# Kernel tuning notes

Hardware: AMD Instinct MI355X
Metric: run time of the kernel (lower is better)

Reference implementation:

```python
import jax, jax.numpy as jnp
import numpy as np

N, E, C, K = 50000, 800000, 64, 8
D = C * K  # 512
NEG_SLOPE = 0.01  # torch leaky_relu default


def setup_inputs() -> dict:
    key = jax.random.key(0)
    ks = jax.random.split(key, 6)
    x = jax.random.normal(ks[0], (N, D), dtype=jnp.float32)
    edge_index = jax.random.randint(ks[1], (2, E), 0, N, dtype=jnp.int64)
    conv_W = jax.random.normal(ks[2], (K, C, C), dtype=jnp.float32) * (1.0 / np.sqrt(C))
    conv_b = jax.random.normal(ks[3], (K, C), dtype=jnp.float32) * 0.01
    W1 = jax.random.normal(ks[4], (D, D), dtype=jnp.float32) * (1.0 / np.sqrt(D))
    W2 = jax.random.normal(ks[5], (D, D), dtype=jnp.float32) * (1.0 / np.sqrt(D))
    return {"x": x, "edge_index": edge_index, "conv_W": conv_W,
            "conv_b": conv_b, "W1": W1, "W2": W2}


def _gcn_conv(xk, Wk, bk, src, dst, dinv, n):
    # PyG GCNConv: transform, then symmetric-normalized aggregation with self-loops,
    # then add bias.
    xt = xk @ Wk.T  # [N, C]
    norm = dinv[src] * dinv[dst]  # [E]
    agg = jax.ops.segment_sum(norm[:, None] * xt[src], dst, num_segments=n)
    agg = agg + (dinv * dinv)[:, None] * xt  # self-loop contribution
    return agg + bk


def reference(x, edge_index, conv_W, conv_b, W1, W2):
    n = x.shape[0]
    src, dst = edge_index[0], edge_index[1]
    # degree with self-loops (edge weight 1)
    deg = jax.ops.segment_sum(jnp.ones((E,), x.dtype), dst, num_segments=n) + 1.0
    dinv = deg ** -0.5
    xr = x.reshape(n, C, K)
    zs = [jax.nn.leaky_relu(_gcn_conv(xr[:, :, i], conv_W[i], conv_b[i], src, dst, dinv, n),
                            negative_slope=NEG_SLOPE)
          for i in range(K)]
    z = jnp.concatenate(zs, axis=1)  # [N, D]
    z = jax.nn.leaky_relu(z, negative_slope=NEG_SLOPE)
    # dropout is identity in eval mode (dr=12 is invalid for torch Dropout anyway)
    z_fc1 = z @ W1.T
    z_fc2 = z @ W2.T
    s = jnp.sum(z_fc1.T @ z_fc2, axis=0)  # [D]
    # softmax over axis 0 of a [1, D] tensor (as in the original code)
    gate = jax.nn.softmax((s / jnp.sqrt(jnp.asarray(D, x.dtype)))[None, :], axis=0)
    return z * gate
```

## Files before the change

### kernel.cpp

```cpp
#include <hip/hip_runtime.h>

#define NN 50000
#define EE 800000
#define KK 8
#define DD 512
#define CAP 64
#define FILL_BLOCKS ((EE + 255) / 256)
#define LROW 520

typedef __attribute__((ext_vector_type(8))) short short8;
typedef __attribute__((ext_vector_type(4))) float f32x4;
typedef __attribute__((ext_vector_type(4))) unsigned u32x4;

__device__ __forceinline__ float leaky2(float v) {
    v = (v < 0.0f) ? 0.01f * v : v;
    v = (v < 0.0f) ? 0.01f * v : v;
    return v;
}

__device__ __forceinline__ unsigned short f2bf(float f) {
    unsigned u = __float_as_uint(f);
    u += 0x7fffu + ((u >> 16) & 1u);
    return (unsigned short)(u >> 16);
}
__device__ __forceinline__ float bf_lo(unsigned u) { return __uint_as_float(u << 16); }
__device__ __forceinline__ float bf_hi(unsigned u) { return __uint_as_float(u & 0xffff0000u); }

__device__ __forceinline__ void add8(float acc[8], u32x4 v) {
    acc[0] += bf_lo(v[0]); acc[1] += bf_hi(v[0]);
    acc[2] += bf_lo(v[1]); acc[3] += bf_hi(v[1]);
    acc[4] += bf_lo(v[2]); acc[5] += bf_hi(v[2]);
    acc[6] += bf_lo(v[3]); acc[7] += bf_hi(v[3]);
}

__global__ void k_fill_wconv(const int* __restrict__ ei, int* __restrict__ cursor,
                             unsigned short* __restrict__ bw,
                             const float* __restrict__ W,
                             unsigned short* __restrict__ Wbf) {
    int b = blockIdx.x;
    if (b < FILL_BLOCKS) {
        int e = b * 256 + threadIdx.x;
        if (e < EE) {
            int s = ei[e];
            int d = ei[EE + e];
            int p = atomicAdd(&cursor[d], 1);
            if (p < CAP) bw[(size_t)d * CAP + p] = (unsigned short)s;
        }
    } else {
        int i = (b - FILL_BLOCKS) * 256 + threadIdx.x;
        if (i < KK * 64 * 64) Wbf[i] = f2bf(W[i]);
    }
}

__global__ __launch_bounds__(256) void k_transform(const float* __restrict__ x,
                                                   const unsigned short* __restrict__ Wbf,
                                                   const int* __restrict__ cnt,
                                                   unsigned short* __restrict__ xt) {
    __shared__ unsigned short lxT[32 * LROW];
    const int t = threadIdx.x;
    const int n0 = blockIdx.x * 32;

    const f32x4* x4 = (const f32x4*)x;
    #pragma unroll
    for (int i = 0; i < 16; i++) {
        int idx = i * 256 + t;
        int n = idx >> 7;
        int q = idx & 127;
        int n_eff = n0 + n; if (n_eff >= NN) n_eff = NN - 1;
        f32x4 v = __builtin_nontemporal_load(&x4[(size_t)n_eff * 128 + q]);
        int c = q >> 1;
        int k0 = (q & 1) * 4;
        unsigned short* p = &lxT[n * LROW + k0 * 64 + c];
        p[0] = f2bf(v[0]); p[64] = f2bf(v[1]); p[128] = f2bf(v[2]); p[192] = f2bf(v[3]);
    }
    __syncthreads();

    const int wv   = t >> 6;
    const int lane = t & 63;
    const int l15  = lane & 15;
    const int quad = lane >> 4;
    const f32x4 zero = {0.f, 0.f, 0.f, 0.f};

    #pragma unroll
    for (int kk = 0; kk < 2; kk++) {
        const int k = wv * 2 + kk;
        short8 afr[4][2];
        #pragma unroll
        for (int jt = 0; jt < 4; jt++)
            #pragma unroll
            for (int ks = 0; ks < 2; ks++)
                afr[jt][ks] = *(const short8*)&Wbf[k * 4096 + (jt * 16 + l15) * 64 + ks * 32 + quad * 8];

        #pragma unroll
        for (int ng = 0; ng < 2; ng++) {
            short8 bfr[2];
            #pragma unroll
            for (int ks = 0; ks < 2; ks++)
                bfr[ks] = *(const short8*)&lxT[(ng * 16 + l15) * LROW + k * 64 + ks * 32 + quad * 8];
            f32x4 acc[4];
            #pragma unroll
            for (int jt = 0; jt < 4; jt++) {
                acc[jt] = zero;
                acc[jt] = __builtin_amdgcn_mfma_f32_16x16x32_bf16(afr[jt][0], bfr[0], acc[jt], 0, 0, 0);
                acc[jt] = __builtin_amdgcn_mfma_f32_16x16x32_bf16(afr[jt][1], bfr[1], acc[jt], 0, 0, 0);
            }
            const int row = ng * 16 + l15;
            int nc = n0 + row; if (nc >= NN) nc = NN - 1;
            const float dv = rsqrtf((float)cnt[nc] + 1.0f);
            #pragma unroll
            for (int jt = 0; jt < 4; jt++) {
                ushort4 h;
                h.x = f2bf(acc[jt][0] * dv); h.y = f2bf(acc[jt][1] * dv);
                h.z = f2bf(acc[jt][2] * dv); h.w = f2bf(acc[jt][3] * dv);
                *(ushort4*)&lxT[row * LROW + k * 64 + jt * 16 + quad * 4] = h;
            }
        }
    }
    __syncthreads();

    #pragma unroll
    for (int i = 0; i < 8; i++) {
        int idx = i * 256 + t;
        int row = idx >> 6;
        int col8 = (idx & 63) * 8;
        int node = n0 + row;
        if (node < NN) {
            u32x4 v = *(const u32x4*)&lxT[row * LROW + col8];
            *(u32x4*)&xt[(size_t)node * DD + col8] = v;
        }
    }
}

__global__ __launch_bounds__(256) void k_agg(const unsigned short* __restrict__ xt,
                                             const int* __restrict__ cursor,
                                             const unsigned short* __restrict__ bw,
                                             const float* __restrict__ bias,
                                             float* __restrict__ out) {
    const int n = __builtin_amdgcn_readfirstlane(blockIdx.x * 4 + (threadIdx.x >> 6));
    const int lane = threadIdx.x & 63;
    const int cnr = cursor[n];
    const float dn = rsqrtf((float)cnr + 1.0f);
    const int cn = cnr > CAP ? CAP : cnr;

    const u32x4* xt4 = (const u32x4*)xt;
    int bidx = (int)bw[(size_t)n * CAP + lane];
    u32x4 a = xt4[((size_t)n << 6) + lane];

    float acc[8];
    acc[0] = bf_lo(a[0]); acc[1] = bf_hi(a[0]);
    acc[2] = bf_lo(a[1]); acc[3] = bf_hi(a[1]);
    acc[4] = bf_lo(a[2]); acc[5] = bf_hi(a[2]);
    acc[6] = bf_lo(a[3]); acc[7] = bf_hi(a[3]);

    int i = 0;
    for (; i + 3 < cn; i += 4) {
        int s0 = __builtin_amdgcn_readlane(bidx, i);
        int s1 = __builtin_amdgcn_readlane(bidx, i + 1);
        int s2 = __builtin_amdgcn_readlane(bidx, i + 2);
        int s3 = __builtin_amdgcn_readlane(bidx, i + 3);
        u32x4 v0 = xt4[((size_t)s0 << 6) + lane];
        u32x4 v1 = xt4[((size_t)s1 << 6) + lane];
        u32x4 v2 = xt4[((size_t)s2 << 6) + lane];
        u32x4 v3 = xt4[((size_t)s3 << 6) + lane];
        __builtin_amdgcn_sched_barrier(0);
        add8(acc, v0); add8(acc, v1); add8(acc, v2); add8(acc, v3);
    }
    if (i + 1 < cn) {
        int s0 = __builtin_amdgcn_readlane(bidx, i);
        int s1 = __builtin_amdgcn_readlane(bidx, i + 1);
        u32x4 v0 = xt4[((size_t)s0 << 6) + lane];
        u32x4 v1 = xt4[((size_t)s1 << 6) + lane];
        add8(acc, v0); add8(acc, v1);
        i += 2;
    }
    if (i < cn) {
        int s0 = __builtin_amdgcn_readlane(bidx, i);
        u32x4 v0 = xt4[((size_t)s0 << 6) + lane];
        add8(acc, v0);
    }

    const float4* b4 = (const float4*)bias;
    float4 b0 = b4[lane * 2], b1 = b4[lane * 2 + 1];
    f32x4 r0, r1;
    r0[0] = leaky2(dn * acc[0] + b0.x); r0[1] = leaky2(dn * acc[1] + b0.y);
    r0[2] = leaky2(dn * acc[2] + b0.z); r0[3] = leaky2(dn * acc[3] + b0.w);
    r1[0] = leaky2(dn * acc[4] + b1.x); r1[1] = leaky2(dn * acc[5] + b1.y);
    r1[2] = leaky2(dn * acc[6] + b1.z); r1[3] = leaky2(dn * acc[7] + b1.w);
    f32x4* o4 = (f32x4*)(out + (size_t)n * DD);
    __builtin_nontemporal_store(r0, o4 + lane * 2);
    __builtin_nontemporal_store(r1, o4 + lane * 2 + 1);
}

extern "C" void kernel_launch(void* const* d_in, const int* in_sizes, int n_in,
                              void* d_out, int out_size, void* d_ws, size_t ws_size,
                              hipStream_t stream) {
    const float* x  = (const float*)d_in[0];
    const int*   ei = (const int*)d_in[1];
    const float* W  = (const float*)d_in[2];
    const float* b  = (const float*)d_in[3];
    float* out = (float*)d_out;

    unsigned short* xt = (unsigned short*)d_ws;
    int* cursor = (int*)(xt + (size_t)NN * DD);
    unsigned short* bw = (unsigned short*)(cursor + NN);
    unsigned short* wbf = bw + (size_t)NN * CAP;

    hipMemsetAsync(cursor, 0, NN * sizeof(int), stream);
    k_fill_wconv<<<FILL_BLOCKS + 128, 256, 0, stream>>>(ei, cursor, bw, W, wbf);
    k_transform<<<(NN + 31) / 32, 256, 0, stream>>>(x, wbf, cursor, xt);
    k_agg<<<NN / 4, 256, 0, stream>>>(xt, cursor, bw, b, out);
}
```

Before: 362.2 us.

## Fuse edge bucketing with feature transform and move source normalization to aggregation

Merges the edge-bucketing kernel and the per-channel transform kernel into one launch, where transform blocks run alongside fill blocks. This is possible because the source-degree scaling no longer happens inside the transform. Each transform block now converts W to bf16 in registers itself, so the separate Wbf pass goes away. In aggregation, each lane looks up its neighbour's degree, and the resulting weight is broadcast with readlane and applied as an FMA. The cost is more work per edge in aggregation, a larger fused kernel holding shared memory even for fill blocks, and redundant W conversion in every transform block.

```diff
diff --git a/kernel.cpp b/kernel.cpp
--- a/kernel.cpp
+++ b/kernel.cpp
@@ -5,6 +5,7 @@
 #define KK 8
 #define DD 512
 #define CAP 64
+#define TR_BLOCKS   ((NN + 31) / 32)
 #define FILL_BLOCKS ((EE + 255) / 256)
 #define LROW 520
 
@@ -26,38 +27,32 @@
 __device__ __forceinline__ float bf_lo(unsigned u) { return __uint_as_float(u << 16); }
 __device__ __forceinline__ float bf_hi(unsigned u) { return __uint_as_float(u & 0xffff0000u); }
 
-__device__ __forceinline__ void add8(float acc[8], u32x4 v) {
-    acc[0] += bf_lo(v[0]); acc[1] += bf_hi(v[0]);
-    acc[2] += bf_lo(v[1]); acc[3] += bf_hi(v[1]);
-    acc[4] += bf_lo(v[2]); acc[5] += bf_hi(v[2]);
-    acc[6] += bf_lo(v[3]); acc[7] += bf_hi(v[3]);
-}
-
-__global__ void k_fill_wconv(const int* __restrict__ ei, int* __restrict__ cursor,
-                             unsigned short* __restrict__ bw,
-                             const float* __restrict__ W,
-                             unsigned short* __restrict__ Wbf) {
-    int b = blockIdx.x;
-    if (b < FILL_BLOCKS) {
-        int e = b * 256 + threadIdx.x;
+__device__ __forceinline__ void fma8(float acc[8], float w, u32x4 v) {
+    acc[0] += w * bf_lo(v[0]); acc[1] += w * bf_hi(v[0]);
+    acc[2] += w * bf_lo(v[1]); acc[3] += w * bf_hi(v[1]);
+    acc[4] += w * bf_lo(v[2]); acc[5] += w * bf_hi(v[2]);
+    acc[6] += w * bf_lo(v[3]); acc[7] += w * bf_hi(v[3]);
+}
+
+__global__ __launch_bounds__(256) void k_fill_transform(
+        const int* __restrict__ ei, int* __restrict__ cursor,
+        unsigned short* __restrict__ bw,
+        const float* __restrict__ x, const float* __restrict__ W,
+        unsigned short* __restrict__ xt) {
+    __shared__ unsigned short lxT[32 * LROW];
+    const int t = threadIdx.x;
+
+    if (blockIdx.x >= TR_BLOCKS) {
+        int e = (blockIdx.x - TR_BLOCKS) * 256 + t;
         if (e < EE) {
             int s = ei[e];
             int d = ei[EE + e];
             int p = atomicAdd(&cursor[d], 1);
             if (p < CAP) bw[(size_t)d * CAP + p] = (unsigned short)s;
         }
-    } else {
-        int i = (b - FILL_BLOCKS) * 256 + threadIdx.x;
-        if (i < KK * 64 * 64) Wbf[i] = f2bf(W[i]);
-    }
-}
-
-__global__ __launch_bounds__(256) void k_transform(const float* __restrict__ x,
-                                                   const unsigned short* __restrict__ Wbf,
-                                                   const int* __restrict__ cnt,
-                                                   unsigned short* __restrict__ xt) {
-    __shared__ unsigned short lxT[32 * LROW];
-    const int t = threadIdx.x;
+        return;
+    }
+
     const int n0 = blockIdx.x * 32;
 
     const f32x4* x4 = (const f32x4*)x;
@@ -80,6 +75,7 @@
     const int l15  = lane & 15;
     const int quad = lane >> 4;
     const f32x4 zero = {0.f, 0.f, 0.f, 0.f};
+    const f32x4* W4 = (const f32x4*)W;
 
     #pragma unroll
     for (int kk = 0; kk < 2; kk++) {
@@ -88,8 +84,16 @@
         #pragma unroll
         for (int jt = 0; jt < 4; jt++)
             #pragma unroll
-            for (int ks = 0; ks < 2; ks++)
-                afr[jt][ks] = *(const short8*)&Wbf[k * 4096 + (jt * 16 + l15) * 64 + ks * 32 + quad * 8];
+            for (int ks = 0; ks < 2; ks++) {
+                int off = (k * 4096 + (jt * 16 + l15) * 64 + ks * 32 + quad * 8) >> 2;
+                f32x4 wa = W4[off], wb = W4[off + 1];
+                short8 f;
+                f[0] = (short)f2bf(wa[0]); f[1] = (short)f2bf(wa[1]);
+                f[2] = (short)f2bf(wa[2]); f[3] = (short)f2bf(wa[3]);
+                f[4] = (short)f2bf(wb[0]); f[5] = (short)f2bf(wb[1]);
+                f[6] = (short)f2bf(wb[2]); f[7] = (short)f2bf(wb[3]);
+                afr[jt][ks] = f;
+            }
 
         #pragma unroll
         for (int ng = 0; ng < 2; ng++) {
@@ -105,13 +109,11 @@
                 acc[jt] = __builtin_amdgcn_mfma_f32_16x16x32_bf16(afr[jt][1], bfr[1], acc[jt], 0, 0, 0);
             }
             const int row = ng * 16 + l15;
-            int nc = n0 + row; if (nc >= NN) nc = NN - 1;
-            const float dv = rsqrtf((float)cnt[nc] + 1.0f);
             #pragma unroll
             for (int jt = 0; jt < 4; jt++) {
                 ushort4 h;
-                h.x = f2bf(acc[jt][0] * dv); h.y = f2bf(acc[jt][1] * dv);
-                h.z = f2bf(acc[jt][2] * dv); h.w = f2bf(acc[jt][3] * dv);
+                h.x = f2bf(acc[jt][0]); h.y = f2bf(acc[jt][1]);
+                h.z = f2bf(acc[jt][2]); h.w = f2bf(acc[jt][3]);
                 *(ushort4*)&lxT[row * LROW + k * 64 + jt * 16 + quad * 4] = h;
             }
         }
@@ -144,14 +146,17 @@
 
     const u32x4* xt4 = (const u32x4*)xt;
     int bidx = (int)bw[(size_t)n * CAP + lane];
+    int sidx = lane < cn ? bidx : 0;
+    float wl = rsqrtf((float)cursor[sidx] + 1.0f);
     u32x4 a = xt4[((size_t)n << 6) + lane];
 
     float acc[8];
-    acc[0] = bf_lo(a[0]); acc[1] = bf_hi(a[0]);
-    acc[2] = bf_lo(a[1]); acc[3] = bf_hi(a[1]);
-    acc[4] = bf_lo(a[2]); acc[5] = bf_hi(a[2]);
-    acc[6] = bf_lo(a[3]); acc[7] = bf_hi(a[3]);
-
+    acc[0] = dn * bf_lo(a[0]); acc[1] = dn * bf_hi(a[0]);
+    acc[2] = dn * bf_lo(a[1]); acc[3] = dn * bf_hi(a[1]);
+    acc[4] = dn * bf_lo(a[2]); acc[5] = dn * bf_hi(a[2]);
+    acc[6] = dn * bf_lo(a[3]); acc[7] = dn * bf_hi(a[3]);
+
+    #define WLANE(i) __uint_as_float(__builtin_amdgcn_readlane(__float_as_uint(wl), (i)))
     int i = 0;
     for (; i + 3 < cn; i += 4) {
         int s0 = __builtin_amdgcn_readlane(bidx, i);
@@ -163,21 +168,23 @@
         u32x4 v2 = xt4[((size_t)s2 << 6) + lane];
         u32x4 v3 = xt4[((size_t)s3 << 6) + lane];
         __builtin_amdgcn_sched_barrier(0);
-        add8(acc, v0); add8(acc, v1); add8(acc, v2); add8(acc, v3);
+        fma8(acc, WLANE(i), v0); fma8(acc, WLANE(i + 1), v1);
+        fma8(acc, WLANE(i + 2), v2); fma8(acc, WLANE(i + 3), v3);
     }
     if (i + 1 < cn) {
         int s0 = __builtin_amdgcn_readlane(bidx, i);
         int s1 = __builtin_amdgcn_readlane(bidx, i + 1);
         u32x4 v0 = xt4[((size_t)s0 << 6) + lane];
         u32x4 v1 = xt4[((size_t)s1 << 6) + lane];
-        add8(acc, v0); add8(acc, v1);
+        fma8(acc, WLANE(i), v0); fma8(acc, WLANE(i + 1), v1);
         i += 2;
     }
     if (i < cn) {
         int s0 = __builtin_amdgcn_readlane(bidx, i);
         u32x4 v0 = xt4[((size_t)s0 << 6) + lane];
-        add8(acc, v0);
-    }
+        fma8(acc, WLANE(i), v0);
+    }
+    #undef WLANE
 
     const float4* b4 = (const float4*)bias;
     float4 b0 = b4[lane * 2], b1 = b4[lane * 2 + 1];
@@ -203,10 +210,8 @@
     unsigned short* xt = (unsigned short*)d_ws;
     int* cursor = (int*)(xt + (size_t)NN * DD);
     unsigned short* bw = (unsigned short*)(cursor + NN);
-    unsigned short* wbf = bw + (size_t)NN * CAP;
 
     hipMemsetAsync(cursor, 0, NN * sizeof(int), stream);
-    k_fill_wconv<<<FILL_BLOCKS + 128, 256, 0, stream>>>(ei, cursor, bw, W, wbf);
-    k_transform<<<(NN + 31) / 32, 256, 0, stream>>>(x, wbf, cursor, xt);
+    k_fill_transform<<<TR_BLOCKS + FILL_BLOCKS, 256, 0, stream>>>(ei, cursor, bw, x, W, xt);
     k_agg<<<NN / 4, 256, 0, stream>>>(xt, cursor, bw, b, out);
 }
```

Result: slower. 380.6 us (+5.1%).
